# Optimization experiments

Hardware: AMD Instinct MI355X
Metric: run time of the kernel (lower is better)

## Reference

```python
import jax, jax.numpy as jnp
import numpy as np

BATCH, SEQ, DIM = 4, 2048, 1024
HEADS = 16
HD = DIM // HEADS  # 64
BASE = 10000.0


def setup_inputs() -> dict:
    key = jax.random.key(0)
    k1, k2, k3 = jax.random.split(key, 3)
    x = jax.random.normal(k1, (BATCH, SEQ, DIM), dtype=jnp.float32)
    # torch Linear weight is (out,in); we store transposed (in,out) so y = x @ w
    w_qkv = jax.random.normal(k2, (DIM, 3 * DIM), dtype=jnp.float32) * (DIM ** -0.5)
    w_out = jax.random.normal(k3, (DIM, DIM), dtype=jnp.float32) * (DIM ** -0.5)
    return {"x": x, "w_qkv": w_qkv, "w_out": w_out}


def _rope_cos_sin(seq_len: int, head_dim: int):
    inv_freq = 1.0 / (BASE ** (jnp.arange(0, head_dim, 2, dtype=jnp.float32) / head_dim))
    t = jnp.arange(seq_len, dtype=jnp.float32)
    freqs = t[:, None] * inv_freq[None, :]          # (S, HD/2)
    emb = jnp.concatenate([freqs, freqs], axis=-1)  # (S, HD)
    return jnp.cos(emb), jnp.sin(emb)


def _rotate_half(x):
    x1, x2 = jnp.split(x, 2, axis=-1)
    return jnp.concatenate([-x2, x1], axis=-1)


def reference(x, w_qkv, w_out):
    B, S, D = x.shape
    qkv = x @ w_qkv                                  # (B,S,3D)
    q, k, v = jnp.split(qkv, 3, axis=-1)
    # (B,S,D) -> (B,H,S,HD)
    q = q.reshape(B, S, HEADS, HD).transpose(0, 2, 1, 3)
    k = k.reshape(B, S, HEADS, HD).transpose(0, 2, 1, 3)
    v = v.reshape(B, S, HEADS, HD).transpose(0, 2, 1, 3)
    cos, sin = _rope_cos_sin(S, HD)                  # (S,HD), broadcast over B,H
    q = q * cos + _rotate_half(q) * sin
    k = k * cos + _rotate_half(k) * sin
    scale = HD ** -0.5
    scores = jnp.einsum('bhqd,bhkd->bhqk', q, k) * scale  # (B,H,S,S)
    causal = jnp.tril(jnp.ones((S, S), dtype=bool))
    scores = jnp.where(causal, scores, -jnp.inf)
    attn = jax.nn.softmax(scores, axis=-1)
    out = jnp.einsum('bhqk,bhkd->bhqd', attn, v)     # (B,H,S,HD)
    out = out.transpose(0, 2, 1, 3).reshape(B, S, D)
    out = out @ w_out
    return out, k, v
```

## Files before the change

kernel.cpp:

```cpp
#include <hip/hip_runtime.h>
#include <hip/hip_bf16.h>
#include <stdint.h>

#define BATCH 4
#define SEQ 2048
#define DIM 1024
#define HEADS 16
#define HD 64
#define BH (BATCH*HEADS)
#define NQKV (3*DIM)

typedef __attribute__((ext_vector_type(8))) short bf16x8;
typedef __attribute__((ext_vector_type(4))) short bf16x4;
typedef __attribute__((ext_vector_type(4))) float f32x4;
typedef __attribute__((ext_vector_type(16))) float f32x16;
typedef __attribute__((ext_vector_type(4))) unsigned u32x4;

#define MFMA16(a,b,c) __builtin_amdgcn_mfma_f32_16x16x32_bf16(a,b,c,0,0,0)
#define MFMA32(a,b,c) __builtin_amdgcn_mfma_f32_32x32x16_bf16(a,b,c,0,0,0)

__device__ inline short f2bf(float f){
    __hip_bfloat16 h = __float2bfloat16(f);
    return *reinterpret_cast<short*>(&h);
}
__device__ inline float bf2f(short s){
    unsigned u = ((unsigned)(unsigned short)s) << 16;
    float f;
    __builtin_memcpy(&f, &u, 4);
    return f;
}

__global__ void conv_bf16(const float* __restrict__ in, short* __restrict__ out, int n){
    int i = blockIdx.x*blockDim.x + threadIdx.x;
    if (i < n) out[i] = f2bf(in[i]);
}

__global__ void transpose_conv(const float* __restrict__ in, short* __restrict__ out, int R, int C){
    __shared__ float tile[32][33];
    int c0 = blockIdx.x*32, r0 = blockIdx.y*32;
    int tx = threadIdx.x, ty = threadIdx.y;
    #pragma unroll
    for (int dy = 0; dy < 32; dy += 8)
        tile[ty+dy][tx] = in[(size_t)(r0+ty+dy)*C + c0+tx];
    __syncthreads();
    #pragma unroll
    for (int dy = 0; dy < 32; dy += 8)
        out[(size_t)(c0+ty+dy)*R + r0+tx] = f2bf(tile[tx][ty+dy]);
}

template<int WRITE_BF16>
__global__ void gemm_bt(const short* __restrict__ A, const short* __restrict__ Bt,
                        void* __restrict__ Cout, int M, int N, int K)
{
    __shared__ short As[128*32];
    __shared__ short Bs[128*32];
    const int t = threadIdx.x;
    const int lane = t & 63, wave = t >> 6;
    const int wr = wave >> 1, wc = wave & 1;
    const int nbn = N >> 7;
    const int bm = blockIdx.x / nbn, bn = blockIdx.x % nbn;
    const int m0 = bm*128, n0 = bn*128;
    const int l15 = lane & 15, lhi = lane >> 4;

    f32x4 acc[4][4];
    #pragma unroll
    for (int i=0;i<4;i++)
        #pragma unroll
        for (int j=0;j<4;j++) acc[i][j] = (f32x4){0.f,0.f,0.f,0.f};

    for (int k0 = 0; k0 < K; k0 += 32) {
        #pragma unroll
        for (int it = 0; it < 2; ++it) {
            int base = (it*256 + wave*64)*8;
            int off  = base + lane*8;
            int row = off >> 5, col = off & 31;
            __builtin_amdgcn_global_load_lds(
                (const __attribute__((address_space(1))) void*)(A + (size_t)(m0+row)*K + k0 + col),
                (__attribute__((address_space(3))) void*)(As + base), 16, 0, 0);
            __builtin_amdgcn_global_load_lds(
                (const __attribute__((address_space(1))) void*)(Bt + (size_t)(n0+row)*K + k0 + col),
                (__attribute__((address_space(3))) void*)(Bs + base), 16, 0, 0);
        }
        __syncthreads();
        bf16x8 a[4], b[4];
        #pragma unroll
        for (int i=0;i<4;i++)
            a[i] = *(const bf16x8*)&As[(wr*64 + i*16 + l15)*32 + lhi*8];
        #pragma unroll
        for (int j=0;j<4;j++)
            b[j] = *(const bf16x8*)&Bs[(wc*64 + j*16 + l15)*32 + lhi*8];
        #pragma unroll
        for (int i=0;i<4;i++)
            #pragma unroll
            for (int j=0;j<4;j++)
                acc[i][j] = MFMA16(a[i], b[j], acc[i][j]);
        __syncthreads();
    }

    #pragma unroll
    for (int i=0;i<4;i++)
        #pragma unroll
        for (int j=0;j<4;j++)
            #pragma unroll
            for (int jj=0;jj<4;jj++) {
                int row = m0 + wr*64 + i*16 + lhi*4 + jj;
                int col = n0 + wc*64 + j*16 + l15;
                if (WRITE_BF16)
                    ((short*)Cout)[(size_t)row*N + col] = f2bf(acc[i][j][jj]);
                else
                    ((float*)Cout)[(size_t)row*N + col] = acc[i][j][jj];
            }
}

__global__ __launch_bounds__(256) void rope_scatter(const short* __restrict__ qkvb,
                             short* __restrict__ qp, short* __restrict__ kp,
                             short* __restrict__ vp,
                             float* __restrict__ kout, float* __restrict__ vout)
{
    __shared__ short vt[64*72];
    const int t = threadIdx.x;
    const int bh = blockIdx.x >> 5;
    const int sb = blockIdx.x & 31;
    const int b = bh >> 4, h = bh & 15;
    const int s_loc = t >> 2, ic = (t & 3) << 3;
    const int s = (sb << 6) + s_loc;
    const size_t rowbase = ((size_t)(b*SEQ + s))*NQKV + h*HD;

    bf16x8 q1 = *(const bf16x8*)&qkvb[rowbase + ic];
    bf16x8 q2 = *(const bf16x8*)&qkvb[rowbase + ic + 32];
    bf16x8 k1 = *(const bf16x8*)&qkvb[rowbase + DIM + ic];
    bf16x8 k2 = *(const bf16x8*)&qkvb[rowbase + DIM + ic + 32];
    bf16x8 v1 = *(const bf16x8*)&qkvb[rowbase + 2*DIM + ic];
    bf16x8 v2 = *(const bf16x8*)&qkvb[rowbase + 2*DIM + ic + 32];

    const float QS = 0.125f * 1.4426950408889634f;
    bf16x8 qo1, qo2, ko1, ko2;
    float k1f[8], k2f[8], v1f[8], v2f[8];
    #pragma unroll
    for (int j=0;j<8;j++){
        int i = ic + j;
        float inv = exp2f(-(float)i * (13.287712379549449f/32.0f));
        float ang = (float)s * inv;
        float sn, cs;
        sincosf(ang, &sn, &cs);
        float q1f = bf2f(q1[j]), q2f = bf2f(q2[j]);
        float ka = bf2f(k1[j]), kb_ = bf2f(k2[j]);
        float qr1 = q1f*cs - q2f*sn, qr2 = q2f*cs + q1f*sn;
        float kr1 = ka*cs - kb_*sn,  kr2 = kb_*cs + ka*sn;
        qo1[j] = f2bf(qr1*QS); qo2[j] = f2bf(qr2*QS);
        ko1[j] = f2bf(kr1);    ko2[j] = f2bf(kr2);
        k1f[j] = kr1; k2f[j] = kr2;
        v1f[j] = bf2f(v1[j]); v2f[j] = bf2f(v2[j]);
    }

    const size_t obase = ((size_t)bh*SEQ + s)*HD;
    #pragma unroll
    for (int j4=0;j4<2;j4++){
        *(f32x4*)&kout[obase+ic+j4*4]    = (f32x4){k1f[j4*4],k1f[j4*4+1],k1f[j4*4+2],k1f[j4*4+3]};
        *(f32x4*)&kout[obase+ic+32+j4*4] = (f32x4){k2f[j4*4],k2f[j4*4+1],k2f[j4*4+2],k2f[j4*4+3]};
        *(f32x4*)&vout[obase+ic+j4*4]    = (f32x4){v1f[j4*4],v1f[j4*4+1],v1f[j4*4+2],v1f[j4*4+3]};
        *(f32x4*)&vout[obase+ic+32+j4*4] = (f32x4){v2f[j4*4],v2f[j4*4+1],v2f[j4*4+2],v2f[j4*4+3]};
    }

    {
        const int tkv = (sb << 1) + (s_loc >> 5);
        const int rlo = s_loc & 31;
        const int g1 = ic >> 3,   i1 = g1 >> 1, H1 = g1 & 1;
        const int g2 = 4+(ic>>3), i2 = g2 >> 1, H2 = g2 & 1;
        const size_t tb = ((size_t)bh*64 + tkv)*4;
        *(bf16x8*)&qp[(tb + i1)*512 + (H1*32 + rlo)*8] = qo1;
        *(bf16x8*)&qp[(tb + i2)*512 + (H2*32 + rlo)*8] = qo2;
        *(bf16x8*)&kp[(tb + i1)*512 + (H1*32 + rlo)*8] = ko1;
        *(bf16x8*)&kp[(tb + i2)*512 + (H2*32 + rlo)*8] = ko2;
    }

    #pragma unroll
    for (int j=0;j<8;j++){
        int i = ic + j;
        vt[i*72 + ((((s_loc>>3) ^ (i&7) ^ (i>>3)) & 7)<<3) + (s_loc&7)] = v1[j];
        int i2 = i + 32;
        vt[i2*72 + ((((s_loc>>3) ^ (i2&7) ^ (i2>>3)) & 7)<<3) + (s_loc&7)] = v2[j];
    }
    __syncthreads();

    const int i_out = t >> 2, g = t & 3;
    const int nn = i_out >> 5, l31v = i_out & 31;
    #pragma unroll
    for (int cc=0; cc<2; ++cc){
        int c = 2*g + cc;
        bf16x8 rv = *(const bf16x8*)&vt[i_out*72 + ((((c) ^ (i_out&7) ^ (i_out>>3)) & 7)<<3)];
        int tkv = (sb << 1) + (c >> 2);
        int m = (c >> 1) & 1, H = c & 1;
        size_t va = ((((size_t)bh*64 + tkv)*2 + nn)*2 + m)*512 + (H*32 + l31v)*8;
        *(bf16x8*)&vp[va] = rv;
    }
}

__global__ __launch_bounds__(64) void attn_partial(
        const short* __restrict__ qp, const short* __restrict__ kp,
        const short* __restrict__ vp, short* __restrict__ obuf,
        float* __restrict__ lbuf)
{
    const int lane = threadIdx.x;
    const int wg = blockIdx.x;
    const int x = wg & 7;
    const int r = wg >> 3;
    const int half = r & 1;
    const int pp = (r >> 1) & 31;
    const int bh = (x << 3) | (r >> 6);
    const int l31 = lane & 31;
    const int H = lane >> 5;
    const short* kbase = kp + (size_t)bh * 64 * 2048;
    const short* vbase = vp + (size_t)bh * 64 * 2048;
    const short* qbase = qp + (size_t)bh * 64 * 2048;

    #pragma unroll 1
    for (int part = 0; part < 2; ++part) {
        const int qt = part ? (63 - pp) : pp;
        const int q0 = qt << 5;
        const int n  = qt + 1;
        const int mid = (n + 1) >> 1;
        const int lo = half ? mid : 0;
        const int hi = half ? n : mid;

        bf16x8 qf[4];
        #pragma unroll
        for (int i=0;i<4;i++)
            qf[i] = *(const bf16x8*)&qbase[((size_t)qt*4 + i)*512 + lane*8];

        f32x16 o[2];
        #pragma unroll
        for (int nn=0;nn<2;nn++)
            #pragma unroll
            for (int rr=0;rr<16;rr++) o[nn][rr] = 0.f;
        float lsum = 0.f;

        bf16x8 kf[4];
        #pragma unroll
        for (int i=0;i<4;i++)
            kf[i] = *(const bf16x8*)&kbase[((size_t)lo*4 + i)*512 + lane*8];

        #pragma unroll 1
        for (int step = lo; step < hi; ++step) {
            const int kv0 = step << 5;

            bf16x8 kn[4];
            if (step + 1 < hi) {
                #pragma unroll
                for (int i=0;i<4;i++)
                    kn[i] = *(const bf16x8*)&kbase[((size_t)(step+1)*4 + i)*512 + lane*8];
            }
            bf16x8 vf[2][2];
            #pragma unroll
            for (int nn=0;nn<2;nn++)
                #pragma unroll
                for (int m=0;m<2;m++)
                    vf[nn][m] = *(const bf16x8*)&vbase[((size_t)step*4 + nn*2 + m)*512 + lane*8];

            __builtin_amdgcn_s_setprio(1);
            f32x16 sacc;
            #pragma unroll
            for (int rr=0;rr<16;rr++) sacc[rr] = 0.f;
            #pragma unroll
            for (int i=0;i<4;i++)
                sacc = MFMA32(kf[i], qf[i], sacc);
            __builtin_amdgcn_s_setprio(0);

            if (step == n-1) {
                #pragma unroll
                for (int rr=0;rr<16;rr++){
                    int kv = kv0 + (rr&3) + 8*(rr>>2) + 4*H;
                    int q  = q0 + l31;
                    if (kv > q) sacc[rr] = -3.0e38f;
                }
            }

            float p[16];
            #pragma unroll
            for (int rr=0;rr<16;rr++){
                p[rr] = exp2f(sacc[rr]);
                lsum += p[rr];
            }

            unsigned W[8], Pp[8];
            #pragma unroll
            for (int j=0;j<8;j++)
                W[j] = (unsigned)(unsigned short)f2bf(p[2*j])
                     | ((unsigned)(unsigned short)f2bf(p[2*j+1]) << 16);
            #pragma unroll
            for (int j=0;j<8;j++)
                Pp[j] = __shfl_xor(W[j], 32);

            u32x4 paw[2];
            #pragma unroll
            for (int m=0;m<2;m++)
                #pragma unroll
                for (int w=0;w<4;w++){
                    int j0 = (w&1) + 4*m;
                    unsigned c0 = (w<2) ? W[j0]    : Pp[j0];
                    unsigned c1 = (w<2) ? Pp[j0+2] : W[j0+2];
                    paw[m][w] = H ? c1 : c0;
                }
            bf16x8 pa[2];
            __builtin_memcpy(&pa[0], &paw[0], 16);
            __builtin_memcpy(&pa[1], &paw[1], 16);

            __builtin_amdgcn_s_setprio(1);
            #pragma unroll
            for (int nn=0;nn<2;nn++)
                #pragma unroll
                for (int m=0;m<2;m++)
                    o[nn] = MFMA32(pa[m], vf[nn][m], o[nn]);
            __builtin_amdgcn_s_setprio(0);

            if (step + 1 < hi) {
                #pragma unroll
                for (int i=0;i<4;i++) kf[i] = kn[i];
            }
        }

        short* ob = obuf + (size_t)(((bh << 6) | qt)*2 + half) * 2048;
        #pragma unroll
        for (int nn=0;nn<2;nn++)
            #pragma unroll
            for (int rr=0;rr<16;rr++){
                int qloc = (rr&3) + 8*(rr>>2) + 4*H;
                ob[qloc*64 + nn*32 + l31] = f2bf(o[nn][rr]);
            }
        lsum += __shfl_xor(lsum, 32);
        float* lb = lbuf + (size_t)(((bh << 6) | qt)*2 + half) * 32;
        if (lane < 32) lb[l31] = lsum;
    }
}

__global__ __launch_bounds__(256) void attn_combine(const short* __restrict__ obuf,
                                                    const float* __restrict__ lbuf,
                                                    short* __restrict__ aob)
{
    const int t = threadIdx.x;
    const int tile = blockIdx.x;
    const int bh = tile >> 6, qt = tile & 63;
    const int b = bh >> 4, h = bh & 15;
    const int q0 = qt << 5;
    const short* o0 = obuf + (size_t)(tile*2) * 2048;
    const short* o1 = o0 + 2048;
    const float* lb = lbuf + (size_t)(tile*2) * 32;
    const int row = t >> 3, c0 = (t & 7) << 3;

    float inv = 1.0f / (lb[row] + lb[32 + row]);
    bf16x8 a = *(const bf16x8*)&o0[row*64 + c0];
    bf16x8 bq = *(const bf16x8*)&o1[row*64 + c0];
    bf16x8 ov;
    #pragma unroll
    for (int j=0;j<8;j++)
        ov[j] = f2bf((bf2f(a[j]) + bf2f(bq[j])) * inv);
    *(bf16x8*)&aob[((size_t)(b*SEQ + q0 + row))*DIM + h*HD + c0] = ov;
}

extern "C" void kernel_launch(void* const* d_in, const int* in_sizes, int n_in,
                              void* d_out, int out_size, void* d_ws, size_t ws_size,
                              hipStream_t stream) {
    const float* x     = (const float*)d_in[0];
    const float* w_qkv = (const float*)d_in[1];
    const float* w_out = (const float*)d_in[2];
    float* out  = (float*)d_out;
    float* kout = out + (size_t)BATCH*SEQ*DIM;
    float* vout = kout + (size_t)BH*SEQ*HD;

    char* ws = (char*)d_ws;
    short* xb    = (short*)(ws + 0);
    short* wqkvT = (short*)(ws + 16777216);
    short* woutT = (short*)(ws + 23068672);
    short* qkvb  = (short*)(ws + 25165824);
    short* obuf  = (short*)(ws + 25165824);
    float* lbuf  = (float*)(ws + 25165824 + 33554432);
    short* qp    = (short*)(ws + 75497472);
    short* kp    = (short*)(ws + 92274688);
    short* vp    = (short*)(ws + 109051904);
    short* aob   = (short*)(ws + 125829120);

    conv_bf16<<<(BATCH*SEQ*DIM)/256, 256, 0, stream>>>(x, xb, BATCH*SEQ*DIM);
    transpose_conv<<<dim3(NQKV/32, DIM/32), dim3(32,8), 0, stream>>>(w_qkv, wqkvT, DIM, NQKV);
    transpose_conv<<<dim3(DIM/32, DIM/32), dim3(32,8), 0, stream>>>(w_out, woutT, DIM, DIM);

    gemm_bt<1><<<(8192/128)*(NQKV/128), 256, 0, stream>>>(xb, wqkvT, qkvb, 8192, NQKV, DIM);

    rope_scatter<<<BH*(SEQ/64), 256, 0, stream>>>(qkvb, qp, kp, vp, kout, vout);

    attn_partial<<<4096, 64, 0, stream>>>(qp, kp, vp, obuf, lbuf);
    attn_combine<<<4096, 256, 0, stream>>>(obuf, lbuf, aob);

    gemm_bt<0><<<(8192/128)*(DIM/128), 256, 0, stream>>>(aob, woutT, out, 8192, DIM, DIM);
}
```

Measured before the change: 237.4 us.

## Software-pipeline attention QK^T, compute row sums via MFMA, swizzle GEMM blocks

The attention inner loop is restructured so the QK^T MFMAs for the next KV tile are issued alongside the exp/pack/PV work of the current tile, using two ping-pong score accumulators. This aims to hide MFMA latency behind the softmax VALU work. Per-row softmax denominators are now accumulated with an extra MFMA against a ones vector instead of scalar adds and a cross-lane shuffle, which trades added matrix work for fewer VALU ops and uses the bf16-rounded probabilities in the sum. The GEMM block index is also remapped in groups of eight, changing which tiles neighbouring blocks process for cache locality.

Result: slower. 262.2 us (+10.5%).

```diff
diff --git a/kernel.cpp b/kernel.cpp
--- a/kernel.cpp
+++ b/kernel.cpp
@@ -58,7 +58,9 @@
     const int lane = t & 63, wave = t >> 6;
     const int wr = wave >> 1, wc = wave & 1;
     const int nbn = N >> 7;
-    const int bm = blockIdx.x / nbn, bn = blockIdx.x % nbn;
+    const int cpx = gridDim.x >> 3;
+    const int swz = (blockIdx.x & 7) * cpx + (blockIdx.x >> 3);
+    const int bm = swz / nbn, bn = swz % nbn;
     const int m0 = bm*128, n0 = bn*128;
     const int l15 = lane & 15, lhi = lane >> 4;
 
@@ -195,6 +197,69 @@
         *(bf16x8*)&vp[va] = rv;
     }
 }
+
+#define ASTEP(SA, SB) do { \
+    const int kv0_ = step << 5; \
+    const bool more_ = (step + 1 < hi); \
+    if (more_) { \
+        _Pragma("unroll") \
+        for (int i=0;i<4;i++) \
+            kf[i] = *(const bf16x8*)&kbase[((size_t)(step+1)*4 + i)*512 + lane*8]; \
+    } \
+    bf16x8 vf[2][2]; \
+    _Pragma("unroll") \
+    for (int nn=0;nn<2;nn++) \
+        _Pragma("unroll") \
+        for (int m=0;m<2;m++) \
+            vf[nn][m] = *(const bf16x8*)&vbase[((size_t)step*4 + nn*2 + m)*512 + lane*8]; \
+    if (step == n-1) { \
+        _Pragma("unroll") \
+        for (int rr=0;rr<16;rr++){ \
+            int kv_ = kv0_ + (rr&3) + 8*(rr>>2) + 4*H; \
+            if (kv_ > q0 + l31) SA[rr] = -3.0e38f; \
+        } \
+    } \
+    float pv_[16]; \
+    _Pragma("unroll") \
+    for (int rr=0;rr<16;rr++) pv_[rr] = exp2f(SA[rr]); \
+    unsigned W_[8], Pp_[8]; \
+    _Pragma("unroll") \
+    for (int j=0;j<8;j++) \
+        W_[j] = (unsigned)(unsigned short)f2bf(pv_[2*j]) \
+              | ((unsigned)(unsigned short)f2bf(pv_[2*j+1]) << 16); \
+    _Pragma("unroll") \
+    for (int j=0;j<8;j++) Pp_[j] = __shfl_xor(W_[j], 32); \
+    u32x4 paw_[2]; \
+    _Pragma("unroll") \
+    for (int m=0;m<2;m++) \
+        _Pragma("unroll") \
+        for (int w=0;w<4;w++){ \
+            int j0_ = (w&1) + 4*m; \
+            unsigned c0_ = (w<2) ? W_[j0_]    : Pp_[j0_]; \
+            unsigned c1_ = (w<2) ? Pp_[j0_+2] : W_[j0_+2]; \
+            paw_[m][w] = H ? c1_ : c0_; \
+        } \
+    bf16x8 pa_[2]; \
+    __builtin_memcpy(&pa_[0], &paw_[0], 16); \
+    __builtin_memcpy(&pa_[1], &paw_[1], 16); \
+    if (more_) { \
+        _Pragma("unroll") \
+        for (int rr=0;rr<16;rr++) SB[rr] = 0.f; \
+        __builtin_amdgcn_s_setprio(1); \
+        _Pragma("unroll") \
+        for (int i=0;i<4;i++) SB = MFMA32(kf[i], qf[i], SB); \
+        __builtin_amdgcn_s_setprio(0); \
+    } \
+    __builtin_amdgcn_s_setprio(1); \
+    _Pragma("unroll") \
+    for (int nn=0;nn<2;nn++) \
+        _Pragma("unroll") \
+        for (int m=0;m<2;m++) \
+            o[nn] = MFMA32(pa_[m], vf[nn][m], o[nn]); \
+    psum = MFMA32(pa_[0], onesf, psum); \
+    psum = MFMA32(pa_[1], onesf, psum); \
+    __builtin_amdgcn_s_setprio(0); \
+} while(0)
 
 __global__ __launch_bounds__(64) void attn_partial(
         const short* __restrict__ qp, const short* __restrict__ kp,
@@ -214,6 +279,10 @@
     const short* vbase = vp + (size_t)bh * 64 * 2048;
     const short* qbase = qp + (size_t)bh * 64 * 2048;
 
+    bf16x8 onesf;
+    #pragma unroll
+    for (int j=0;j<8;j++) onesf[j] = (short)0x3F80;
+
     #pragma unroll 1
     for (int part = 0; part < 2; ++part) {
         const int qt = part ? (63 - pp) : pp;
@@ -228,94 +297,33 @@
         for (int i=0;i<4;i++)
             qf[i] = *(const bf16x8*)&qbase[((size_t)qt*4 + i)*512 + lane*8];
 
-        f32x16 o[2];
+        f32x16 o[2], psum;
         #pragma unroll
         for (int nn=0;nn<2;nn++)
             #pragma unroll
             for (int rr=0;rr<16;rr++) o[nn][rr] = 0.f;
-        float lsum = 0.f;
-
-        bf16x8 kf[4];
-        #pragma unroll
-        for (int i=0;i<4;i++)
-            kf[i] = *(const bf16x8*)&kbase[((size_t)lo*4 + i)*512 + lane*8];
-
-        #pragma unroll 1
-        for (int step = lo; step < hi; ++step) {
-            const int kv0 = step << 5;
-
-            bf16x8 kn[4];
-            if (step + 1 < hi) {
-                #pragma unroll
-                for (int i=0;i<4;i++)
-                    kn[i] = *(const bf16x8*)&kbase[((size_t)(step+1)*4 + i)*512 + lane*8];
-            }
-            bf16x8 vf[2][2];
-            #pragma unroll
-            for (int nn=0;nn<2;nn++)
-                #pragma unroll
-                for (int m=0;m<2;m++)
-                    vf[nn][m] = *(const bf16x8*)&vbase[((size_t)step*4 + nn*2 + m)*512 + lane*8];
-
+        #pragma unroll
+        for (int rr=0;rr<16;rr++) psum[rr] = 0.f;
+
+        if (lo < hi) {
+            bf16x8 kf[4];
+            #pragma unroll
+            for (int i=0;i<4;i++)
+                kf[i] = *(const bf16x8*)&kbase[((size_t)lo*4 + i)*512 + lane*8];
+            f32x16 s0, s1;
+            #pragma unroll
+            for (int rr=0;rr<16;rr++) s0[rr] = 0.f;
             __builtin_amdgcn_s_setprio(1);
-            f32x16 sacc;
-            #pragma unroll
-            for (int rr=0;rr<16;rr++) sacc[rr] = 0.f;
-            #pragma unroll
-            for (int i=0;i<4;i++)
-                sacc = MFMA32(kf[i], qf[i], sacc);
+            #pragma unroll
+            for (int i=0;i<4;i++) s0 = MFMA32(kf[i], qf[i], s0);
             __builtin_amdgcn_s_setprio(0);
 
-            if (step == n-1) {
-                #pragma unroll
-                for (int rr=0;rr<16;rr++){
-                    int kv = kv0 + (rr&3) + 8*(rr>>2) + 4*H;
-                    int q  = q0 + l31;
-                    if (kv > q) sacc[rr] = -3.0e38f;
-                }
-            }
-
-            float p[16];
-            #pragma unroll
-            for (int rr=0;rr<16;rr++){
-                p[rr] = exp2f(sacc[rr]);
-                lsum += p[rr];
-            }
-
-            unsigned W[8], Pp[8];
-            #pragma unroll
-            for (int j=0;j<8;j++)
-                W[j] = (unsigned)(unsigned short)f2bf(p[2*j])
-                     | ((unsigned)(unsigned short)f2bf(p[2*j+1]) << 16);
-            #pragma unroll
-            for (int j=0;j<8;j++)
-                Pp[j] = __shfl_xor(W[j], 32);
-
-            u32x4 paw[2];
-            #pragma unroll
-            for (int m=0;m<2;m++)
-                #pragma unroll
-                for (int w=0;w<4;w++){
-                    int j0 = (w&1) + 4*m;
-                    unsigned c0 = (w<2) ? W[j0]    : Pp[j0];
-                    unsigned c1 = (w<2) ? Pp[j0+2] : W[j0+2];
-                    paw[m][w] = H ? c1 : c0;
-                }
-            bf16x8 pa[2];
-            __builtin_memcpy(&pa[0], &paw[0], 16);
-            __builtin_memcpy(&pa[1], &paw[1], 16);
-
-            __builtin_amdgcn_s_setprio(1);
-            #pragma unroll
-            for (int nn=0;nn<2;nn++)
-                #pragma unroll
-                for (int m=0;m<2;m++)
-                    o[nn] = MFMA32(pa[m], vf[nn][m], o[nn]);
-            __builtin_amdgcn_s_setprio(0);
-
-            if (step + 1 < hi) {
-                #pragma unroll
-                for (int i=0;i<4;i++) kf[i] = kn[i];
+            int step = lo;
+            while (1) {
+                ASTEP(s0, s1);
+                ++step; if (step >= hi) break;
+                ASTEP(s1, s0);
+                ++step; if (step >= hi) break;
             }
         }
 
@@ -327,11 +335,17 @@
                 int qloc = (rr&3) + 8*(rr>>2) + 4*H;
                 ob[qloc*64 + nn*32 + l31] = f2bf(o[nn][rr]);
             }
-        lsum += __shfl_xor(lsum, 32);
         float* lb = lbuf + (size_t)(((bh << 6) | qt)*2 + half) * 32;
-        if (lane < 32) lb[l31] = lsum;
-    }
-}
+        if (l31 == 0) {
+            #pragma unroll
+            for (int rr=0;rr<16;rr++){
+                int qloc = (rr&3) + 8*(rr>>2) + 4*H;
+                lb[qloc] = psum[rr];
+            }
+        }
+    }
+}
+#undef ASTEP
 
 __global__ __launch_bounds__(256) void attn_combine(const short* __restrict__ obuf,
                                                     const float* __restrict__ lbuf,
```
